# Kernel tuning notes

Measured on AMD Instinct MI355X. Metric: run time of the kernel, lower is better.

Reference implementation:

```python
import jax, jax.numpy as jnp
import numpy as np

EMB_DIM = 2048
N_HEADS = 16
HEAD_DIM = EMB_DIM // N_HEADS
B, S = 4, 2048


def setup_inputs() -> dict:
    key = jax.random.key(0)
    kx, kq, kk, kv, ko = jax.random.split(key, 5)
    scale = 0.02
    return {
        "x": jax.random.normal(kx, (B, S, EMB_DIM), dtype=jnp.float32),
        "Wq": jax.random.normal(kq, (EMB_DIM, EMB_DIM), dtype=jnp.float32) * scale,
        "Wk": jax.random.normal(kk, (EMB_DIM, EMB_DIM), dtype=jnp.float32) * scale,
        "Wv": jax.random.normal(kv, (EMB_DIM, EMB_DIM), dtype=jnp.float32) * scale,
        "Wo": jax.random.normal(ko, (EMB_DIM, EMB_DIM), dtype=jnp.float32) * scale,
        "bo": jnp.zeros((EMB_DIM,), dtype=jnp.float32),
    }


def _split_heads(t):
    # [B, S, E] -> [B, H, S, Dh]
    b, s, _ = t.shape
    return t.reshape(b, s, N_HEADS, HEAD_DIM).transpose(0, 2, 1, 3)


def reference(x, Wq, Wk, Wv, Wo, bo):
    # torch nn.Linear: y = x @ W.T (no bias for qkv, bias for out_proj)
    q = _split_heads(x @ Wq.T)  # [B, H, S, Dh]
    k = _split_heads(x @ Wk.T)
    v = _split_heads(x @ Wv.T)

    scores = jnp.einsum("bhqd,bhkd->bhqk", q, k)  # [B, H, S, S]
    q_pos = jnp.arange(S)
    k_pos = jnp.arange(S)
    causal_mask = q_pos[:, None] < k_pos[None, :]  # True => future token, masked
    scores = jnp.where(causal_mask, -jnp.inf, scores)
    attn = jax.nn.softmax(scores / np.sqrt(HEAD_DIM).astype(np.float32), axis=-1)
    # dropout rate 0 (eval) -> identity
    ctx = jnp.einsum("bhqk,bhkd->bhqd", attn, v)  # [B, H, S, Dh]
    ctx = ctx.transpose(0, 2, 1, 3).reshape(B, S, EMB_DIM)
    return ctx @ Wo.T + bo
```

## Files before the change

kernel.cpp:

```cpp
#include <hip/hip_runtime.h>
#include <math.h>

#define EMB 2048
#define HD 128
#define SEQ 2048
#define MTOT 8192

typedef __bf16 bf16x8 __attribute__((ext_vector_type(8)));
typedef float floatx4 __attribute__((ext_vector_type(4)));

__device__ __forceinline__ unsigned short f2bf(float f) {
    unsigned u = __float_as_uint(f);
    return (unsigned short)((u + 0x7FFFu + ((u >> 16) & 1u)) >> 16);
}

__device__ __forceinline__ void gl_lds16(const void* g, void* lds) {
    __builtin_amdgcn_global_load_lds(
        (const __attribute__((address_space(1))) unsigned int*)g,
        (__attribute__((address_space(3))) unsigned int*)lds,
        16, 0, 0);
}

__global__ void cast_all_kernel(const float* __restrict__ x,
                                const float* __restrict__ w0,
                                const float* __restrict__ w1,
                                const float* __restrict__ w2,
                                const float* __restrict__ w3,
                                unsigned short* __restrict__ xb,
                                unsigned short* __restrict__ wb0,
                                unsigned short* __restrict__ wb1,
                                unsigned short* __restrict__ wb2,
                                unsigned short* __restrict__ wb3)
{
    const int XN4 = MTOT * EMB / 4;
    const int WN4 = EMB * EMB / 4;
    int i = blockIdx.x * blockDim.x + threadIdx.x;
    const float* src; unsigned short* dst; int off;
    if (i < XN4) { src = x; dst = xb; off = i; }
    else {
        int j = i - XN4;
        int wsel = j >> 20;
        off = j & (WN4 - 1);
        switch (wsel) {
            case 0: src = w0; dst = wb0; break;
            case 1: src = w1; dst = wb1; break;
            case 2: src = w2; dst = wb2; break;
            default: src = w3; dst = wb3; break;
        }
    }
    float4 v = reinterpret_cast<const float4*>(src)[off];
    ushort4 o;
    o.x = f2bf(v.x); o.y = f2bf(v.y); o.z = f2bf(v.z); o.w = f2bf(v.w);
    reinterpret_cast<ushort4*>(dst)[off] = o;
}


#define PH_PRE()  do { asm volatile("s_barrier" ::: "memory");               \
                       asm volatile("s_waitcnt lgkmcnt(0)" ::: "memory");    \
                       __builtin_amdgcn_sched_barrier(0);                    \
                       __builtin_amdgcn_s_setprio(1); } while (0)
#define PH_POST() do { __builtin_amdgcn_s_setprio(0);                        \
                       asm volatile("s_barrier" ::: "memory"); } while (0)

#define MFMA16(AF, BF, MI0)                                                  \
    _Pragma("unroll")                                                        \
    for (int mi = 0; mi < 4; mi++)                                           \
        _Pragma("unroll")                                                    \
        for (int ni = 0; ni < 4; ni++)                                       \
            acc[(MI0) + mi][ni] = __builtin_amdgcn_mfma_f32_16x16x32_bf16(   \
                AF[(MI0) + mi], BF[ni], acc[(MI0) + mi][ni], 0, 0, 0);

#define KTILE(BUF, S1, S2, S3, S4, VM)                                       \
  do {                                                                       \
    bf16x8 a0[8], b0[4];                                                     \
    _Pragma("unroll")                                                        \
    for (int mi = 0; mi < 8; mi++)                                           \
        a0[mi] = *reinterpret_cast<const bf16x8*>(baA[BUF][0] + mi * 2048);  \
    _Pragma("unroll")                                                        \
    for (int ni = 0; ni < 4; ni++)                                           \
        b0[ni] = *reinterpret_cast<const bf16x8*>(baB[BUF][0] + ni * 2048);  \
    STAGE(S1);                                                               \
    asm volatile("s_waitcnt lgkmcnt(8)" ::: "memory");                       \
    PH_PRE();                                                                \
    MFMA16(a0, b0, 0);                                                       \
    PH_POST();                                                               \
    bf16x8 a1[8];                                                            \
    _Pragma("unroll")                                                        \
    for (int mi = 0; mi < 8; mi++)                                           \
        a1[mi] = *reinterpret_cast<const bf16x8*>(baA[BUF][1] + mi * 2048);  \
    STAGE(S2);                                                               \
    PH_PRE();                                                                \
    MFMA16(a0, b0, 4);                                                       \
    PH_POST();                                                               \
    bf16x8 b1[4];                                                            \
    _Pragma("unroll")                                                        \
    for (int ni = 0; ni < 4; ni++)                                           \
        b1[ni] = *reinterpret_cast<const bf16x8*>(baB[BUF][1] + ni * 2048);  \
    STAGE(S3);                                                               \
    PH_PRE();                                                                \
    MFMA16(a1, b1, 0);                                                       \
    PH_POST();                                                               \
    STAGE(S4);                                                               \
    asm volatile("s_waitcnt " VM ::: "memory");                              \
    PH_PRE();                                                                \
    MFMA16(a1, b1, 4);                                                       \
    PH_POST();                                                               \
  } while (0)

template<bool OUT_F32>
__global__ __launch_bounds__(512, 2)
void gemm256_bt(const unsigned short* __restrict__ A,
                const unsigned short* __restrict__ Bw0,
                const unsigned short* __restrict__ Bw1,
                const unsigned short* __restrict__ Bw2,
                void* __restrict__ Cout0,
                void* __restrict__ Cout1,
                void* __restrict__ Cout2,
                const float* __restrict__ bias,
                int M, int N, int K, float scale0)
{
    __shared__ __align__(16) unsigned short sA[2][256][64];
    __shared__ __align__(16) unsigned short sB[2][256][64];

    const unsigned short* Bw = (blockIdx.z == 0) ? Bw0 : (blockIdx.z == 1) ? Bw1 : Bw2;
    void* Cout = (blockIdx.z == 0) ? Cout0 : (blockIdx.z == 1) ? Cout1 : Cout2;
    const float osc = (blockIdx.z == 0) ? scale0 : 1.0f;

    const int tid  = threadIdx.x;
    const int lane = tid & 63;
    const int wave = tid >> 6;
    const int wm   = wave >> 2;
    const int wn   = wave & 3;
    const int col  = lane & 15;
    const int quad = lane >> 4;

    const int m0 = blockIdx.y * 256;
    const int n0 = blockIdx.x * 256;

    const int NT     = K >> 6;
    const int NITER  = NT >> 1;
    const int fourNT = NT << 2;

    int off[2];
    #pragma unroll
    for (int q = 0; q < 2; q++) {
        int P = (tid + (q << 9)) << 4;
        int r = P >> 7;
        int c = ((P & 127) ^ ((r & 7) << 4)) >> 1;
        off[q] = r * K + c;
    }

    const int X = (col & 7) << 4;
    const char* baA[2][2];
    const char* baB[2][2];
    #pragma unroll
    for (int buf = 0; buf < 2; buf++)
        #pragma unroll
        for (int kk = 0; kk < 2; kk++) {
            int sw = (((kk << 6) | (quad << 4)) ^ X);
            baA[buf][kk] = (const char*)&sA[buf][0][0] + (wm << 14) + (col << 7) + sw;
            baB[buf][kk] = (const char*)&sB[buf][0][0] + (wn << 13) + (col << 7) + sw;
        }

    floatx4 acc[8][4];
    #pragma unroll
    for (int i = 0; i < 8; i++)
        #pragma unroll
        for (int j = 0; j < 4; j++)
            #pragma unroll
            for (int r = 0; r < 4; r++) acc[i][j][r] = 0.0f;

    auto STAGE = [&](int s) {
        if (s >= fourNT) return;
        int t = s >> 2, j = s & 3;
        int buf = t & 1;
        int k0 = t << 6;
        int jrow = (j & 1) << 7;
        const unsigned short* src = (j < 2) ? A : Bw;
        int urow = ((j < 2) ? m0 : n0) + jrow;
        const unsigned short* gp = src + (size_t)urow * K + k0;
        unsigned short* region = (j < 2) ? &sA[buf][jrow][0] : &sB[buf][jrow][0];
        char* ldsb = (char*)region + (wave << 10);
        #pragma unroll
        for (int q = 0; q < 2; q++)
            gl_lds16(gp + off[q], ldsb + (q << 13));
    };

    #pragma unroll
    for (int s = 0; s < 6; s++) STAGE(s);
    asm volatile("s_waitcnt vmcnt(4)" ::: "memory");
    asm volatile("s_barrier" ::: "memory");

    #pragma unroll 1
    for (int it = 0; it < NITER - 1; ++it) {
        const int sb = 5 + (it << 3);
        KTILE(0, sb + 1, sb + 2, sb + 3, sb + 4, "vmcnt(4)");
        KTILE(1, sb + 5, sb + 6, sb + 7, sb + 8, "vmcnt(4)");
    }
    {
        const int sb = 5 + ((NITER - 1) << 3);
        KTILE(0, sb + 1, sb + 2, sb + 3, sb + 4, "vmcnt(0)");
        KTILE(1, sb + 5, sb + 6, sb + 7, sb + 8, "vmcnt(4)");
    }

    #pragma unroll
    for (int mi = 0; mi < 8; mi++) {
        #pragma unroll
        for (int ni = 0; ni < 4; ni++) {
            #pragma unroll
            for (int r = 0; r < 4; r++) {
                int row = m0 + (wm << 7) + (mi << 4) + (quad << 2) + r;
                int cg  = n0 + (wn << 6) + (ni << 4) + col;
                float v = acc[mi][ni][r];
                if (OUT_F32) {
                    float bb = bias ? bias[cg] : 0.0f;
                    reinterpret_cast<float*>(Cout)[(size_t)row * N + cg] = v + bb;
                } else {
                    reinterpret_cast<unsigned short*>(Cout)[(size_t)row * N + cg] = f2bf(v * osc);
                }
            }
        }
    }
}

__global__ __launch_bounds__(256, 2)
void flash_attn(const unsigned short* __restrict__ Q,
                const unsigned short* __restrict__ Kg,
                const unsigned short* __restrict__ Vg,
                unsigned short* __restrict__ O)
{
    __shared__ __align__(16) unsigned short sK[64 * 128];
    __shared__ __align__(16) unsigned short sVt[128][72];
    __shared__ __align__(16) unsigned short sP[4][16 * 72];

    const int tid  = threadIdx.x;
    const int lane = tid & 63;
    const int w    = tid >> 6;
    const int col  = lane & 15;
    const int quad = lane >> 4;

    const int h = blockIdx.y;
    const int b = blockIdx.z;
    const size_t rowbase = (size_t)b * SEQ;
    const int hoff = h * HD;

    unsigned short* sPw = sP[w];

    const int vk4 = (tid & 15) * 4;
    const int vd0 = (tid >> 4) * 8;

    #pragma unroll
    for (int phase = 0; phase < 2; phase++) {
        const int qsb = phase ? (int)blockIdx.x : (SEQ/128 - 1) - (int)blockIdx.x;
        const int qbase = qsb * 128;
        const int qg0 = qbase + w*32 + col;
        const int qg1 = qg0 + 16;

        bf16x8 qf[2][4];
        {
            const unsigned short* qr0 = Q + (rowbase + qg0) * EMB + hoff;
            const unsigned short* qr1 = Q + (rowbase + qg1) * EMB + hoff;
            #pragma unroll
            for (int ks = 0; ks < 4; ks++) {
                qf[0][ks] = *reinterpret_cast<const bf16x8*>(qr0 + ks*32 + quad*8);
                qf[1][ks] = *reinterpret_cast<const bf16x8*>(qr1 + ks*32 + quad*8);
            }
        }

        floatx4 oacc[2][8];
        #pragma unroll
        for (int g = 0; g < 2; g++)
            #pragma unroll
            for (int ni = 0; ni < 8; ni++)
                #pragma unroll
                for (int r = 0; r < 4; r++) oacc[g][ni][r] = 0.0f;
        float l_i[2] = {0.0f, 0.0f};

        const int ktmax = qbase / 64 + 1;
        for (int kt = 0; kt <= ktmax; kt++) {
            const int k0 = kt * 64;
            #pragma unroll
            for (int i = 0; i < 4; i++) {
                int c = tid + i * 256;
                int key = c >> 4;
                int dblk = (c & 15) ^ (key & 7);
                char* ldsK = (char*)sK + (size_t)(i * 256 + w * 64) * 16;
                gl_lds16(Kg + (rowbase + k0 + key) * EMB + hoff + dblk * 8, ldsK);
            }
            {
                unsigned short va[4][8];
                #pragma unroll
                for (int kk = 0; kk < 4; kk++)
                    *reinterpret_cast<int4*>(va[kk]) =
                        *reinterpret_cast<const int4*>(Vg + (rowbase + k0 + vk4 + kk) * EMB + hoff + vd0);
                #pragma unroll
                for (int j = 0; j < 8; j++) {
                    ushort4 o;
                    o.x = va[0][j]; o.y = va[1][j]; o.z = va[2][j]; o.w = va[3][j];
                    *reinterpret_cast<ushort4*>(&sVt[vd0 + j][vk4]) = o;
                }
            }
            __syncthreads();

            if (k0 <= qbase + w*32 + 31) {
                floatx4 sc[2][4];
                #pragma unroll
                for (int g = 0; g < 2; g++)
                    #pragma unroll
                    for (int ni = 0; ni < 4; ni++)
                        #pragma unroll
                        for (int r = 0; r < 4; r++) sc[g][ni][r] = 0.0f;
                #pragma unroll
                for (int ni = 0; ni < 4; ni++) {
                    #pragma unroll
                    for (int ks = 0; ks < 4; ks++) {
                        int u = (ni*16 + col) * 16 + ((ks*4 + quad) ^ (col & 7));
                        bf16x8 kf = *reinterpret_cast<const bf16x8*>(&sK[u * 8]);
                        sc[0][ni] = __builtin_amdgcn_mfma_f32_16x16x32_bf16(kf, qf[0][ks], sc[0][ni], 0, 0, 0);
                        sc[1][ni] = __builtin_amdgcn_mfma_f32_16x16x32_bf16(kf, qf[1][ks], sc[1][ni], 0, 0, 0);
                    }
                }

                const bool need_mask = (k0 + 63 > qbase + w*32);
                bf16x8 pf[2][2];

                #pragma unroll
                for (int g = 0; g < 2; g++) {
                    const int qg = (g == 0) ? qg0 : qg1;
                    if (need_mask) {
                        #pragma unroll
                        for (int ni = 0; ni < 4; ni++)
                            #pragma unroll
                            for (int r = 0; r < 4; r++) {
                                int key = k0 + ni*16 + quad*4 + r;
                                if (key > qg) sc[g][ni][r] = -1e30f;
                            }
                    }
                    float rsum = 0.0f;
                    #pragma unroll
                    for (int ni = 0; ni < 4; ni++) {
                        float p0 = __expf(sc[g][ni][0]);
                        float p1 = __expf(sc[g][ni][1]);
                        float p2 = __expf(sc[g][ni][2]);
                        float p3 = __expf(sc[g][ni][3]);
                        rsum += (p0 + p1) + (p2 + p3);
                        ushort4 pk;
                        pk.x = f2bf(p0); pk.y = f2bf(p1); pk.z = f2bf(p2); pk.w = f2bf(p3);
                        *reinterpret_cast<ushort4*>(&sPw[col*72 + ni*16 + quad*4]) = pk;
                    }
                    l_i[g] += rsum;
                    #pragma unroll
                    for (int ks = 0; ks < 2; ks++)
                        pf[g][ks] = *reinterpret_cast<const bf16x8*>(&sPw[col*72 + ks*32 + quad*8]);
                }

                #pragma unroll
                for (int ni = 0; ni < 8; ni++) {
                    #pragma unroll
                    for (int ks = 0; ks < 2; ks++) {
                        bf16x8 vf = *reinterpret_cast<const bf16x8*>(&sVt[ni*16 + col][ks*32 + quad*8]);
                        oacc[0][ni] = __builtin_amdgcn_mfma_f32_16x16x32_bf16(vf, pf[0][ks], oacc[0][ni], 0, 0, 0);
                        oacc[1][ni] = __builtin_amdgcn_mfma_f32_16x16x32_bf16(vf, pf[1][ks], oacc[1][ni], 0, 0, 0);
                    }
                }
            }
            __syncthreads();
        }

        #pragma unroll
        for (int g = 0; g < 2; g++) {
            const int qg = (g == 0) ? qg0 : qg1;
            float l = l_i[g];
            l += __shfl_xor(l, 16);
            l += __shfl_xor(l, 32);
            float inv = 1.0f / l;
            #pragma unroll
            for (int ni = 0; ni < 8; ni++) {
                ushort4 o4;
                o4.x = f2bf(oacc[g][ni][0] * inv);
                o4.y = f2bf(oacc[g][ni][1] * inv);
                o4.z = f2bf(oacc[g][ni][2] * inv);
                o4.w = f2bf(oacc[g][ni][3] * inv);
                *reinterpret_cast<ushort4*>(O + (rowbase + qg) * EMB + hoff + ni*16 + quad*4) = o4;
            }
        }
    }
}

extern "C" void kernel_launch(void* const* d_in, const int* in_sizes, int n_in,
                              void* d_out, int out_size, void* d_ws, size_t ws_size,
                              hipStream_t stream)
{
    const float* x  = (const float*)d_in[0];
    const float* Wq = (const float*)d_in[1];
    const float* Wk = (const float*)d_in[2];
    const float* Wv = (const float*)d_in[3];
    const float* Wo = (const float*)d_in[4];
    const float* bo = (const float*)d_in[5];
    float* out = (float*)d_out;

    unsigned short* ws = (unsigned short*)d_ws;
    const size_t XN = (size_t)MTOT * EMB;
    const size_t WN = (size_t)EMB * EMB;
    unsigned short* xb  = ws;
    unsigned short* wqb = xb  + XN;
    unsigned short* wkb = wqb + WN;
    unsigned short* wvb = wkb + WN;
    unsigned short* wob = wvb + WN;
    unsigned short* qb  = wob + WN;
    unsigned short* kb  = qb  + XN;
    unsigned short* vb  = kb  + XN;
    unsigned short* ctx = xb;

    {
        int total4 = (int)(XN/4 + 4*(WN/4));
        cast_all_kernel<<<total4 / 256, 256, 0, stream>>>(
            x, Wq, Wk, Wv, Wo, xb, wqb, wkb, wvb, wob);
    }

    const float scl = 0.08838834764831845f;
    gemm256_bt<false><<<dim3(EMB/256, MTOT/256, 3), 512, 0, stream>>>(
        xb, wqb, wkb, wvb, qb, kb, vb, nullptr, MTOT, EMB, EMB, scl);

    flash_attn<<<dim3(SEQ/128/2, 16, 4), 256, 0, stream>>>(qb, kb, vb, ctx);

    gemm256_bt<true><<<dim3(EMB/256, MTOT/256, 1), 512, 0, stream>>>(
        ctx, wob, nullptr, nullptr, out, nullptr, nullptr, bo, MTOT, EMB, EMB, 1.0f);
}
```

Baseline: 595.7 us.

## Simplify GEMM pipeline to whole-tile prefetch with two MFMA phases per k-tile

Replaces the fine-grained staging schedule, which issued quarter-tile global-to-LDS loads interleaved across four MFMA phases with partial vmcnt waits, with a simpler scheme. The whole next k-tile is issued at the start of each tile, followed by two 32-MFMA phases and a full vmcnt(0) wait plus barrier at the end. This cuts the barriers and lgkmcnt waits per k-tile and makes the code easier to follow. In exchange the prefetch distance shrinks to one tile and the full drain each tile can expose global memory latency.

```diff
diff --git a/kernel.cpp b/kernel.cpp
--- a/kernel.cpp
+++ b/kernel.cpp
@@ -55,12 +55,9 @@
 }
 
 
-#define PH_PRE()  do { asm volatile("s_barrier" ::: "memory");               \
-                       asm volatile("s_waitcnt lgkmcnt(0)" ::: "memory");    \
-                       __builtin_amdgcn_sched_barrier(0);                    \
-                       __builtin_amdgcn_s_setprio(1); } while (0)
-#define PH_POST() do { __builtin_amdgcn_s_setprio(0);                        \
-                       asm volatile("s_barrier" ::: "memory"); } while (0)
+#define BAR()   asm volatile("s_barrier" ::: "memory")
+#define PRIO1() __builtin_amdgcn_s_setprio(1)
+#define PRIO0() __builtin_amdgcn_s_setprio(0)
 
 #define MFMA16(AF, BF, MI0)                                                  \
     _Pragma("unroll")                                                        \
@@ -70,7 +67,7 @@
             acc[(MI0) + mi][ni] = __builtin_amdgcn_mfma_f32_16x16x32_bf16(   \
                 AF[(MI0) + mi], BF[ni], acc[(MI0) + mi][ni], 0, 0, 0);
 
-#define KTILE(BUF, S1, S2, S3, S4, VM)                                       \
+#define TILE2(BUF, G, TS)                                                    \
   do {                                                                       \
     bf16x8 a0[8], b0[4];                                                     \
     _Pragma("unroll")                                                        \
@@ -79,32 +76,27 @@
     _Pragma("unroll")                                                        \
     for (int ni = 0; ni < 4; ni++)                                           \
         b0[ni] = *reinterpret_cast<const bf16x8*>(baB[BUF][0] + ni * 2048);  \
-    STAGE(S1);                                                               \
-    asm volatile("s_waitcnt lgkmcnt(8)" ::: "memory");                       \
-    PH_PRE();                                                                \
+    if (G) STAGE_TILE(TS);                                                   \
+    BAR();                                                                   \
+    PRIO1();                                                                 \
     MFMA16(a0, b0, 0);                                                       \
-    PH_POST();                                                               \
-    bf16x8 a1[8];                                                            \
+    MFMA16(a0, b0, 4);                                                       \
+    PRIO0();                                                                 \
+    BAR();                                                                   \
+    bf16x8 a1[8], b1[4];                                                     \
     _Pragma("unroll")                                                        \
     for (int mi = 0; mi < 8; mi++)                                           \
         a1[mi] = *reinterpret_cast<const bf16x8*>(baA[BUF][1] + mi * 2048);  \
-    STAGE(S2);                                                               \
-    PH_PRE();                                                                \
-    MFMA16(a0, b0, 4);                                                       \
-    PH_POST();                                                               \
-    bf16x8 b1[4];                                                            \
     _Pragma("unroll")                                                        \
     for (int ni = 0; ni < 4; ni++)                                           \
         b1[ni] = *reinterpret_cast<const bf16x8*>(baB[BUF][1] + ni * 2048);  \
-    STAGE(S3);                                                               \
-    PH_PRE();                                                                \
+    BAR();                                                                   \
+    PRIO1();                                                                 \
     MFMA16(a1, b1, 0);                                                       \
-    PH_POST();                                                               \
-    STAGE(S4);                                                               \
-    asm volatile("s_waitcnt " VM ::: "memory");                              \
-    PH_PRE();                                                                \
     MFMA16(a1, b1, 4);                                                       \
-    PH_POST();                                                               \
+    PRIO0();                                                                 \
+    asm volatile("s_waitcnt vmcnt(0)" ::: "memory");                         \
+    BAR();                                                                   \
   } while (0)
 
 template<bool OUT_F32>
@@ -137,9 +129,8 @@
     const int m0 = blockIdx.y * 256;
     const int n0 = blockIdx.x * 256;
 
-    const int NT     = K >> 6;
-    const int NITER  = NT >> 1;
-    const int fourNT = NT << 2;
+    const int NT    = K >> 6;
+    const int NITER = NT >> 1;
 
     int off[2];
     #pragma unroll
@@ -170,37 +161,30 @@
             #pragma unroll
             for (int r = 0; r < 4; r++) acc[i][j][r] = 0.0f;
 
-    auto STAGE = [&](int s) {
-        if (s >= fourNT) return;
-        int t = s >> 2, j = s & 3;
-        int buf = t & 1;
-        int k0 = t << 6;
-        int jrow = (j & 1) << 7;
-        const unsigned short* src = (j < 2) ? A : Bw;
-        int urow = ((j < 2) ? m0 : n0) + jrow;
-        const unsigned short* gp = src + (size_t)urow * K + k0;
-        unsigned short* region = (j < 2) ? &sA[buf][jrow][0] : &sB[buf][jrow][0];
-        char* ldsb = (char*)region + (wave << 10);
-        #pragma unroll
-        for (int q = 0; q < 2; q++)
-            gl_lds16(gp + off[q], ldsb + (q << 13));
+    auto STAGE_TILE = [&](int t) {
+        const int bufo = (t & 1) << 15;
+        const int k0   = t << 6;
+        #pragma unroll
+        for (int j = 0; j < 4; j++) {
+            const unsigned short* src = (j < 2) ? A : Bw;
+            const int urow = ((j < 2) ? m0 : n0) + ((j & 1) << 7);
+            const unsigned short* gp = src + (size_t)urow * K + k0;
+            char* ldsb = ((j < 2) ? (char*)sA : (char*)sB)
+                         + bufo + ((j & 1) << 14) + (wave << 10);
+            #pragma unroll
+            for (int q = 0; q < 2; q++)
+                gl_lds16(gp + off[q], ldsb + (q << 13));
+        }
     };
 
-    #pragma unroll
-    for (int s = 0; s < 6; s++) STAGE(s);
-    asm volatile("s_waitcnt vmcnt(4)" ::: "memory");
-    asm volatile("s_barrier" ::: "memory");
+    STAGE_TILE(0);
+    asm volatile("s_waitcnt vmcnt(0)" ::: "memory");
+    BAR();
 
     #pragma unroll 1
-    for (int it = 0; it < NITER - 1; ++it) {
-        const int sb = 5 + (it << 3);
-        KTILE(0, sb + 1, sb + 2, sb + 3, sb + 4, "vmcnt(4)");
-        KTILE(1, sb + 5, sb + 6, sb + 7, sb + 8, "vmcnt(4)");
-    }
-    {
-        const int sb = 5 + ((NITER - 1) << 3);
-        KTILE(0, sb + 1, sb + 2, sb + 3, sb + 4, "vmcnt(0)");
-        KTILE(1, sb + 5, sb + 6, sb + 7, sb + 8, "vmcnt(4)");
+    for (int it = 0; it < NITER; ++it) {
+        TILE2(0, true,            2 * it + 1);
+        TILE2(1, it < NITER - 1,  2 * it + 2);
     }
 
     #pragma unroll
```

Result: slower. 650.3 us (+9.2%).

## Double-buffer K/V tiles in flash attention and remap GEMM blocks across XCDs

Applied to the files above, without the earlier changes.

The flash attention loop now double-buffers K and V in LDS. It prefetches the next K tile via global_load_lds and the next V tile into registers before computing the current tile, then writes V to the alternate buffer after compute. This removes one barrier per iteration and overlaps global loads with MFMA work. The GEMM kernel also remaps block indices so that consecutive XCD-assigned blocks share M rows, aiming for better L2 reuse. The cost is more LDS (roughly 70KB per block), which may limit occupancy under launch_bounds(256,2), plus more live registers. The remap hardcodes an 8x32 grid.

```diff
diff --git a/kernel.cpp b/kernel.cpp
--- a/kernel.cpp
+++ b/kernel.cpp
@@ -134,12 +134,19 @@
     const int col  = lane & 15;
     const int quad = lane >> 4;
 
-    const int m0 = blockIdx.y * 256;
-    const int n0 = blockIdx.x * 256;
-
-    const int NT     = K >> 6;
-    const int NITER  = NT >> 1;
-    const int fourNT = NT << 2;
+    int bx = blockIdx.x, by = blockIdx.y;
+    {
+        int lin = by * 8 + bx;
+        int xcd = lin & 7, k = lin >> 3;
+        bx = k & 7;
+        by = xcd + ((k >> 3) << 3);
+    }
+
+    const int m0 = by * 256;
+    const int n0 = bx * 256;
+
+    const int NT    = K >> 6;
+    const int NITER = NT >> 1;
 
     int off[2];
     #pragma unroll
@@ -171,7 +178,7 @@
             for (int r = 0; r < 4; r++) acc[i][j][r] = 0.0f;
 
     auto STAGE = [&](int s) {
-        if (s >= fourNT) return;
+        if (s >= (NT << 2)) return;
         int t = s >> 2, j = s & 3;
         int buf = t & 1;
         int k0 = t << 6;
@@ -229,8 +236,8 @@
                 const unsigned short* __restrict__ Vg,
                 unsigned short* __restrict__ O)
 {
-    __shared__ __align__(16) unsigned short sK[64 * 128];
-    __shared__ __align__(16) unsigned short sVt[128][72];
+    __shared__ __align__(16) unsigned short sK[2][64 * 128];
+    __shared__ __align__(16) unsigned short sVt[2][128][72];
     __shared__ __align__(16) unsigned short sP[4][16 * 72];
 
     const int tid  = threadIdx.x;
@@ -248,6 +255,33 @@
 
     const int vk4 = (tid & 15) * 4;
     const int vd0 = (tid >> 4) * 8;
+
+    auto stageK = [&](int kt, int buf) {
+        const int k0 = kt * 64;
+        #pragma unroll
+        for (int i = 0; i < 4; i++) {
+            int c = tid + i * 256;
+            int key = c >> 4;
+            int dblk = (c & 15) ^ (key & 7);
+            char* ldsK = (char*)sK[buf] + (size_t)(i * 256 + w * 64) * 16;
+            gl_lds16(Kg + (rowbase + k0 + key) * EMB + hoff + dblk * 8, ldsK);
+        }
+    };
+    auto loadV = [&](int kt, unsigned short (&va)[4][8]) {
+        const int k0 = kt * 64;
+        #pragma unroll
+        for (int kk = 0; kk < 4; kk++)
+            *reinterpret_cast<int4*>(va[kk]) =
+                *reinterpret_cast<const int4*>(Vg + (rowbase + k0 + vk4 + kk) * EMB + hoff + vd0);
+    };
+    auto writeV = [&](unsigned short (&va)[4][8], int buf) {
+        #pragma unroll
+        for (int j = 0; j < 8; j++) {
+            ushort4 o;
+            o.x = va[0][j]; o.y = va[1][j]; o.z = va[2][j]; o.w = va[3][j];
+            *reinterpret_cast<ushort4*>(&sVt[buf][vd0 + j][vk4]) = o;
+        }
+    };
 
     #pragma unroll
     for (int phase = 0; phase < 2; phase++) {
@@ -277,30 +311,21 @@
         float l_i[2] = {0.0f, 0.0f};
 
         const int ktmax = qbase / 64 + 1;
+
+        {
+            unsigned short va[4][8];
+            stageK(0, 0);
+            loadV(0, va);
+            writeV(va, 0);
+            __syncthreads();
+        }
+
         for (int kt = 0; kt <= ktmax; kt++) {
             const int k0 = kt * 64;
-            #pragma unroll
-            for (int i = 0; i < 4; i++) {
-                int c = tid + i * 256;
-                int key = c >> 4;
-                int dblk = (c & 15) ^ (key & 7);
-                char* ldsK = (char*)sK + (size_t)(i * 256 + w * 64) * 16;
-                gl_lds16(Kg + (rowbase + k0 + key) * EMB + hoff + dblk * 8, ldsK);
-            }
-            {
-                unsigned short va[4][8];
-                #pragma unroll
-                for (int kk = 0; kk < 4; kk++)
-                    *reinterpret_cast<int4*>(va[kk]) =
-                        *reinterpret_cast<const int4*>(Vg + (rowbase + k0 + vk4 + kk) * EMB + hoff + vd0);
-                #pragma unroll
-                for (int j = 0; j < 8; j++) {
-                    ushort4 o;
-                    o.x = va[0][j]; o.y = va[1][j]; o.z = va[2][j]; o.w = va[3][j];
-                    *reinterpret_cast<ushort4*>(&sVt[vd0 + j][vk4]) = o;
-                }
-            }
-            __syncthreads();
+            const int cur = kt & 1;
+            const bool have_next = (kt < ktmax);
+            unsigned short va[4][8];
+            if (have_next) { stageK(kt + 1, cur ^ 1); loadV(kt + 1, va); }
 
             if (k0 <= qbase + w*32 + 31) {
                 floatx4 sc[2][4];
@@ -315,7 +340,7 @@
                     #pragma unroll
                     for (int ks = 0; ks < 4; ks++) {
                         int u = (ni*16 + col) * 16 + ((ks*4 + quad) ^ (col & 7));
-                        bf16x8 kf = *reinterpret_cast<const bf16x8*>(&sK[u * 8]);
+                        bf16x8 kf = *reinterpret_cast<const bf16x8*>(&sK[cur][u * 8]);
                         sc[0][ni] = __builtin_amdgcn_mfma_f32_16x16x32_bf16(kf, qf[0][ks], sc[0][ni], 0, 0, 0);
                         sc[1][ni] = __builtin_amdgcn_mfma_f32_16x16x32_bf16(kf, qf[1][ks], sc[1][ni], 0, 0, 0);
                     }
@@ -358,12 +383,14 @@
                 for (int ni = 0; ni < 8; ni++) {
                     #pragma unroll
                     for (int ks = 0; ks < 2; ks++) {
-                        bf16x8 vf = *reinterpret_cast<const bf16x8*>(&sVt[ni*16 + col][ks*32 + quad*8]);
+                        bf16x8 vf = *reinterpret_cast<const bf16x8*>(&sVt[cur][ni*16 + col][ks*32 + quad*8]);
                         oacc[0][ni] = __builtin_amdgcn_mfma_f32_16x16x32_bf16(vf, pf[0][ks], oacc[0][ni], 0, 0, 0);
                         oacc[1][ni] = __builtin_amdgcn_mfma_f32_16x16x32_bf16(vf, pf[1][ks], oacc[1][ni], 0, 0, 0);
                     }
                 }
             }
+
+            if (have_next) writeV(va, cur ^ 1);
             __syncthreads();
         }
 
```

After: 575.3 us. 1.04x faster.
